# Kernel optimization log

Measured on AMD Instinct MI355X. Metric: run time of the kernel, lower is better.

The kernel has to match this reference:

```python
import jax, jax.numpy as jnp
import numpy as np

# dims: batch, tokens, model dim, heads, head_dim, context len, n_blocks, ffn dim
B, L, D, H, HD, S, NB, DFF = 1, 3072, 1024, 16, 64, 512, 2, 4096
T3, H3, W3 = 12, 16, 16  # latent video grid, T3*H3*W3 == L


def _ln(x):
    # LayerNorm, elementwise_affine=False, eps=1e-6
    m = jnp.mean(x, axis=-1, keepdims=True)
    v = jnp.mean(jnp.square(x - m), axis=-1, keepdims=True)
    return (x - m) * jax.lax.rsqrt(v + 1e-6)


def _rot_half(x):
    x1, x2 = jnp.split(x, 2, axis=-1)
    return jnp.concatenate([-x2, x1], axis=-1)


def _rope3d(head_dim, t, h, w):
    d = head_dim // 6
    def band(n):
        freqs = 1.0 / 10000.0 ** (np.arange(0, 2 * d, 2, dtype=np.float32) / (2 * d))
        return np.outer(np.arange(n, dtype=np.float32), freqs)  # [n, d]
    te, he, we = band(t), band(h), band(w)
    rope = np.zeros((t, h, w, head_dim), dtype=np.float32)
    rope[:, :, :, :d] = te[:, None, None, :]
    rope[:, :, :, d:2 * d] = he[None, :, None, :]
    rope[:, :, :, 2 * d:3 * d] = we[None, None, :, :]
    return jnp.asarray(rope.reshape(t * h * w, head_dim))


def _forward(x, timestep_emb, context_emb, rope_emb, adaW, adab, sqW, skW, svW,
             soW, sob, cqW, ckW, cvW, coW, cob, f1W, f1b, f2W, f2b):
    Bv, Lv, Dv = x.shape
    hd = rope_emb.shape[-1]
    nh = Dv // hd
    scale = hd ** -0.5
    cos = jnp.cos(rope_emb)[None, None]  # [1,1,L,hd]
    sin = jnp.sin(rope_emb)[None, None]

    def heads(y):  # [B,N,D] -> [B,H,N,hd]
        return y.reshape(Bv, -1, nh, hd).transpose(0, 2, 1, 3)

    def merge(y):  # [B,H,L,hd] -> [B,L,D]
        return y.transpose(0, 2, 1, 3).reshape(Bv, Lv, Dv)

    for i in range(adaW.shape[0]):
        mods = timestep_emb @ adaW[i].T + adab[i]  # [B, 6D]
        sh_msa, sc_msa, g_msa, sh_mlp, sc_mlp, g_mlp = jnp.split(mods, 6, axis=-1)
        # --- AdaLN + self-attention with RoPE ---
        hx = _ln(x) * (1.0 + sc_msa[:, None, :]) + sh_msa[:, None, :]
        q, k, v = heads(hx @ sqW[i].T), heads(hx @ skW[i].T), heads(hx @ svW[i].T)
        q = q * cos + _rot_half(q) * sin
        k = k * cos + _rot_half(k) * sin
        a = jax.nn.softmax(jnp.einsum('bhld,bhmd->bhlm', q, k) * scale, axis=-1)
        o = merge(jnp.einsum('bhlm,bhmd->bhld', a, v))
        x = x + g_msa[:, None, :] * (o @ soW[i].T + sob[i])
        # --- cross-attention (no gate, no modulation) ---
        hx = _ln(x)
        q = heads(hx @ cqW[i].T)
        k = heads(context_emb @ ckW[i].T)
        v = heads(context_emb @ cvW[i].T)
        a = jax.nn.softmax(jnp.einsum('bhld,bhsd->bhls', q, k) * scale, axis=-1)
        o = merge(jnp.einsum('bhls,bhsd->bhld', a, v))
        x = x + (o @ coW[i].T + cob[i])
        # --- AdaLN + MLP (exact GELU) ---
        hx = _ln(x) * (1.0 + sc_mlp[:, None, :]) + sh_mlp[:, None, :]
        hx = jax.nn.gelu(hx @ f1W[i].T + f1b[i], approximate=False)
        x = x + g_mlp[:, None, :] * (hx @ f2W[i].T + f2b[i])
    return x


def setup_inputs() -> dict:
    ks = jax.random.split(jax.random.key(0), 20)
    s = 0.02
    return {
        'x': jax.random.normal(ks[0], (B, L, D), jnp.float32),
        'timestep_emb': jax.random.normal(ks[1], (B, D), jnp.float32),
        'context_emb': jax.random.normal(ks[2], (B, S, D), jnp.float32),
        'rope_emb': _rope3d(HD, T3, H3, W3),
        'adaW': jax.random.normal(ks[3], (NB, 6 * D, D), jnp.float32) * s,
        'adab': jnp.zeros((NB, 6 * D), jnp.float32),
        'sqW': jax.random.normal(ks[4], (NB, D, D), jnp.float32) * s,
        'skW': jax.random.normal(ks[5], (NB, D, D), jnp.float32) * s,
        'svW': jax.random.normal(ks[6], (NB, D, D), jnp.float32) * s,
        'soW': jax.random.normal(ks[7], (NB, D, D), jnp.float32) * s,
        'sob': jnp.zeros((NB, D), jnp.float32),
        'cqW': jax.random.normal(ks[8], (NB, D, D), jnp.float32) * s,
        'ckW': jax.random.normal(ks[9], (NB, D, D), jnp.float32) * s,
        'cvW': jax.random.normal(ks[10], (NB, D, D), jnp.float32) * s,
        'coW': jax.random.normal(ks[11], (NB, D, D), jnp.float32) * s,
        'cob': jnp.zeros((NB, D), jnp.float32),
        'f1W': jax.random.normal(ks[12], (NB, DFF, D), jnp.float32) * s,
        'f1b': jnp.zeros((NB, DFF), jnp.float32),
        'f2W': jax.random.normal(ks[13], (NB, D, DFF), jnp.float32) * s,
        'f2b': jnp.zeros((NB, D), jnp.float32),
    }


def reference(x, timestep_emb, context_emb, rope_emb, adaW, adab, sqW, skW, svW,
              soW, sob, cqW, ckW, cvW, coW, cob, f1W, f1b, f2W, f2b):
    return _forward(x, timestep_emb, context_emb, rope_emb, adaW, adab, sqW, skW,
                    svW, soW, sob, cqW, ckW, cvW, coW, cob, f1W, f1b, f2W, f2b)
```

## Files before the change

kernel.cpp:

```cpp
#include <hip/hip_runtime.h>
#include <math.h>

typedef __attribute__((ext_vector_type(8))) short bf16x8;
typedef __attribute__((ext_vector_type(4))) float f32x4;
typedef unsigned short u16;
typedef unsigned int u32;

#define DEV static __device__ __forceinline__

typedef __attribute__((address_space(3))) u32 lds_u32;
typedef const __attribute__((address_space(1))) u32 glb_u32;

DEV void gload16(const void* g, void* l){
  __builtin_amdgcn_global_load_lds((glb_u32*)g, (lds_u32*)l, 16, 0, 0);
}

DEV u16 f2bf(float f){
  u32 u = __builtin_bit_cast(u32, f);
  u32 r = (u + 0x7fffu + ((u >> 16) & 1u)) >> 16;
  return (u16)r;
}
DEV float bf2f(u16 h){
  u32 u = ((u32)h) << 16;
  return __builtin_bit_cast(float, u);
}
DEV u32 cvtpk(float a, float b){
  u32 r;
  asm("v_cvt_pk_bf16_f32 %0, %1, %2" : "=v"(r) : "v"(a), "v"(b));
  return r;
}
DEV float gelu_exact(float x){ return 0.5f*x*(1.f+erff(x*0.70710678118654752f)); }

#define QSCALE 0.18033688f

DEV void xcd_remap(int &bx, int &by){
  int gx = gridDim.x, gy = gridDim.y;
  int n = gx*gy;
  if ((n & 7) == 0){
    int id = by*gx + bx;
    int q = n >> 3;
    int sid = (id & 7)*q + (id >> 3);
    bx = sid % gx;
    by = sid / gx;
  }
}

__global__ __launch_bounds__(256) void k_copy_f32(const float* __restrict__ in, float* __restrict__ out, int n4){
  int i = blockIdx.x*256 + threadIdx.x;
  if (i < n4) ((float4*)out)[i] = ((const float4*)in)[i];
}

__global__ __launch_bounds__(256) void k_cvt_bf16(const float* __restrict__ in, u16* __restrict__ out, int n4){
  int i = blockIdx.x*256 + threadIdx.x;
  if (i < n4){
    float4 v = ((const float4*)in)[i];
    ushort4 o;
    o.x = f2bf(v.x); o.y = f2bf(v.y); o.z = f2bf(v.z); o.w = f2bf(v.w);
    ((ushort4*)out)[i] = o;
  }
}

struct CvtArgs { const float4* s[16]; ushort4* d[16]; };
__global__ __launch_bounds__(256) void k_cvt_all(CvtArgs a){
  int i = blockIdx.x*256 + threadIdx.x;
  int seg = i >> 19;
  int off = i & 0x7FFFF;
  float4 v = a.s[seg][off];
  ushort4 o;
  o.x = f2bf(v.x); o.y = f2bf(v.y); o.z = f2bf(v.z); o.w = f2bf(v.w);
  a.d[seg][off] = o;
}

__global__ __launch_bounds__(256) void k_trig(const float* __restrict__ rope,
    float2* __restrict__ ctq, float2* __restrict__ ctk){
  int i = blockIdx.x*256 + threadIdx.x;
  int d = i & 63;
  float a = rope[i];
  float c = cosf(a), s = sinf(a);
  float sg = (d < 32) ? -s : s;
  ctk[i] = make_float2(c, sg);
  ctq[i] = make_float2(c*QSCALE, sg*QSCALE);
}

__global__ __launch_bounds__(256) void k_ada(const float* __restrict__ te,
    const float* __restrict__ adaW, const float* __restrict__ adab,
    float* __restrict__ mods){
  int row = blockIdx.x*4 + (threadIdx.x>>6);
  int lane = threadIdx.x & 63;
  const float* wr = adaW + (size_t)row*1024;
  float s = 0.f;
  #pragma unroll
  for (int j=0; j<4; j++){
    int c = lane*4 + j*256;
    float4 a = *(const float4*)(te + c);
    float4 b = *(const float4*)(wr + c);
    s += a.x*b.x + a.y*b.y + a.z*b.z + a.w*b.w;
  }
  #pragma unroll
  for (int off=32; off; off>>=1) s += __shfl_down(s, off);
  if (!lane) mods[row] = s + adab[row];
}

__global__ __launch_bounds__(256) void k_ln_mod(const float* __restrict__ x,
    const float* __restrict__ sh, const float* __restrict__ sc,
    u16* __restrict__ out){
  int row = blockIdx.x, t = threadIdx.x;
  const float* xr = x + (size_t)row*1024;
  float4 v = ((const float4*)xr)[t];
  float s  = v.x+v.y+v.z+v.w;
  float sq = v.x*v.x+v.y*v.y+v.z*v.z+v.w*v.w;
  #pragma unroll
  for (int off=32; off; off>>=1){ s += __shfl_down(s,off); sq += __shfl_down(sq,off); }
  __shared__ float red[8];
  int w = t>>6, lane = t&63;
  if (!lane){ red[w] = s; red[4+w] = sq; }
  __syncthreads();
  s  = red[0]+red[1]+red[2]+red[3];
  sq = red[4]+red[5]+red[6]+red[7];
  float mean = s*(1.f/1024.f);
  float var  = sq*(1.f/1024.f) - mean*mean;
  float rst  = rsqrtf(var + 1e-6f);
  float vv[4] = {v.x, v.y, v.z, v.w};
  ushort4 o;
  u16 ob[4];
  #pragma unroll
  for (int j=0;j<4;j++){
    int col = t*4+j;
    float y = (vv[j]-mean)*rst;
    if (sh) y = y*(1.f + sc[col]) + sh[col];
    ob[j] = f2bf(y);
  }
  o.x=ob[0]; o.y=ob[1]; o.z=ob[2]; o.w=ob[3];
  *(ushort4*)(out + (size_t)row*1024 + t*4) = o;
}

__global__ __launch_bounds__(256) void k_rope(u16* __restrict__ q, u16* __restrict__ k,
    const float* __restrict__ rope){
  int idx = blockIdx.x*256 + threadIdx.x;
  int d = idx & 31;
  int h = (idx >> 5) & 15;
  int p = idx >> 9;
  const float* rr = rope + (size_t)p*64;
  float a0 = rr[d], a1 = rr[d+32];
  float c0 = cosf(a0), s0 = sinf(a0);
  float c1 = cosf(a1), s1 = sinf(a1);
  size_t o = (size_t)p*1024 + h*64 + d;
  float q0 = bf2f(q[o]), q1 = bf2f(q[o+32]);
  q[o]    = f2bf((q0*c0 - q1*s0)*QSCALE);
  q[o+32] = f2bf((q1*c1 + q0*s1)*QSCALE);
  float k0 = bf2f(k[o]), k1 = bf2f(k[o+32]);
  k[o]    = f2bf(k0*c0 - k1*s0);
  k[o+32] = f2bf(k1*c1 + k0*s1);
}

DEV void gemm_loop(const u16* __restrict__ X, const u16* __restrict__ W,
                   int bm, int bn, int ld, int lenK, u16* As, u16* Bs, f32x4 acc[4][4])
{
  int t = threadIdx.x;
  int w = t>>6, lane = t&63;
  int wr = (w>>1)*64, wc = (w&1)*64;
  int fr = lane&15, g = lane>>4;
  int arow = lane>>2, acol = (lane&3)*8;
  const u16* xp = X + (size_t)(bm + w*32 + arow)*ld + acol;
  const u16* wp = W + (size_t)(bn + w*32 + arow)*ld + acol;
  int nk = lenK >> 5;
  {
    u16* a = As + w*1024; u16* b = Bs + w*1024;
    gload16(xp, a);             gload16(xp + (size_t)16*ld, a + 512);
    gload16(wp, b);             gload16(wp + (size_t)16*ld, b + 512);
  }
  for (int kt = 0; kt < nk; ++kt){
    __syncthreads();
    int cur = kt & 1;
    if (kt + 1 < nk){
      int nb = cur ^ 1;
      int k0 = (kt+1) << 5;
      u16* a = As + nb*4096 + w*1024; u16* b = Bs + nb*4096 + w*1024;
      gload16(xp + k0, a);        gload16(xp + k0 + (size_t)16*ld, a + 512);
      gload16(wp + k0, b);        gload16(wp + k0 + (size_t)16*ld, b + 512);
    }
    const u16* ab = As + cur*4096;
    const u16* bb = Bs + cur*4096;
    bf16x8 a[4], b[4];
    #pragma unroll
    for (int i=0;i<4;i++) a[i] = *(const bf16x8*)(ab + (wr+i*16+fr)*32 + g*8);
    #pragma unroll
    for (int i=0;i<4;i++) b[i] = *(const bf16x8*)(bb + (wc+i*16+fr)*32 + g*8);
    __builtin_amdgcn_s_setprio(1);
    #pragma unroll
    for (int i=0;i<4;i++)
      #pragma unroll
      for (int j=0;j<4;j++)
        acc[i][j] = __builtin_amdgcn_mfma_f32_16x16x32_bf16(a[i], b[j], acc[i][j], 0, 0, 0);
    __builtin_amdgcn_s_setprio(0);
  }
}

template<int EPI>
__global__ __launch_bounds__(256) void k_gemm_bf16(
    const u16* __restrict__ X, const u16* __restrict__ W,
    const float* __restrict__ bias,
    u16* __restrict__ Yout,
    const float* __restrict__ resin, float* __restrict__ resout,
    const float* __restrict__ gate,
    int M, int N, int K)
{
  __shared__ __align__(16) u16 As[2*128*32];
  __shared__ __align__(16) u16 Bs[2*128*32];
  int bx = blockIdx.x, by = blockIdx.y;
  xcd_remap(bx, by);
  int bm = bx*128, bn = by*128;
  f32x4 acc[4][4] = {};
  gemm_loop(X, W, bm, bn, K, K, As, Bs, acc);
  int lane = threadIdx.x & 63, w = threadIdx.x>>6;
  int wr = (w>>1)*64, wc = (w&1)*64;
  int fr = lane&15, g = lane>>4;
  #pragma unroll
  for (int i=0;i<4;i++){
    #pragma unroll
    for (int j=0;j<4;j++){
      int col = bn + wc + j*16 + fr;
      float bv = bias ? bias[col] : 0.f;
      #pragma unroll
      for (int r=0;r<4;r++){
        int row = bm + wr + i*16 + g*4 + r;
        float y = acc[i][j][r] + bv;
        if (EPI == 1){
          Yout[(size_t)row*N + col] = f2bf(gelu_exact(y));
        } else if (EPI == 2){
          float gt = gate ? gate[col] : 1.f;
          resout[(size_t)row*N + col] = resin[(size_t)row*N + col] + gt*y;
        } else {
          Yout[(size_t)row*N + col] = f2bf(y*QSCALE);
        }
      }
    }
  }
}

__global__ __launch_bounds__(256) void k_gemm_part(
    const u16* __restrict__ X, const u16* __restrict__ W,
    float* __restrict__ pp, int M, int N, int K, int Ks)
{
  __shared__ __align__(16) u16 As[2*128*32];
  __shared__ __align__(16) u16 Bs[2*128*32];
  int bx = blockIdx.x, by = blockIdx.y;
  xcd_remap(bx, by);
  int s = blockIdx.z;
  int bm = bx*128, bn = by*128;
  f32x4 acc[4][4] = {};
  gemm_loop(X + (size_t)s*Ks, W + (size_t)s*Ks, bm, bn, K, Ks, As, Bs, acc);
  float* out = pp + (size_t)s*M*N;
  int lane = threadIdx.x & 63, w = threadIdx.x>>6;
  int wr = (w>>1)*64, wc = (w&1)*64;
  int fr = lane&15, g = lane>>4;
  #pragma unroll
  for (int i=0;i<4;i++)
    #pragma unroll
    for (int j=0;j<4;j++){
      int col = bn + wc + j*16 + fr;
      #pragma unroll
      for (int r=0;r<4;r++){
        int row = bm + wr + i*16 + g*4 + r;
        out[(size_t)row*N + col] = acc[i][j][r];
      }
    }
}

template<int EPI>
__global__ __launch_bounds__(256) void k_reduce(
    const float* __restrict__ pp, int S, const float* __restrict__ bias,
    const float* __restrict__ resin, float* __restrict__ resout,
    const float* __restrict__ gate, u16* __restrict__ Ybf,
    int MN, int N)
{
  int idx = blockIdx.x*256 + threadIdx.x;
  int base = idx*4;
  if (base >= MN) return;
  float4 s4 = *(const float4*)(pp + base);
  for (int s=1; s<S; ++s){
    float4 t4 = *(const float4*)(pp + (size_t)s*MN + base);
    s4.x += t4.x; s4.y += t4.y; s4.z += t4.z; s4.w += t4.w;
  }
  int col = base & (N-1);
  float b0=0,b1=0,b2=0,b3=0;
  if (bias){ b0=bias[col]; b1=bias[col+1]; b2=bias[col+2]; b3=bias[col+3]; }
  if (EPI == 2){
    float g0=1,g1=1,g2=1,g3=1;
    if (gate){ g0=gate[col]; g1=gate[col+1]; g2=gate[col+2]; g3=gate[col+3]; }
    float4 rv = *(const float4*)(resin + base);
    float4 o;
    o.x = rv.x + g0*(s4.x+b0);
    o.y = rv.y + g1*(s4.y+b1);
    o.z = rv.z + g2*(s4.z+b2);
    o.w = rv.w + g3*(s4.w+b3);
    *(float4*)(resout + base) = o;
  } else {
    ushort4 o;
    o.x = f2bf((s4.x+b0)*QSCALE);
    o.y = f2bf((s4.y+b1)*QSCALE);
    o.z = f2bf((s4.z+b2)*QSCALE);
    o.w = f2bf((s4.w+b3)*QSCALE);
    *(ushort4*)(Ybf + base) = o;
  }
}

template<int MOD>
__global__ __launch_bounds__(256) void k_reduce_ln(
    const float* __restrict__ pp, int S, const float* __restrict__ bias,
    const float* __restrict__ resin, float* __restrict__ resout,
    const float* __restrict__ gate,
    const float* __restrict__ sh, const float* __restrict__ sc,
    u16* __restrict__ hx)
{
  int row = blockIdx.x, t = threadIdx.x;
  size_t base = (size_t)row*1024 + t*4;
  const size_t MN = (size_t)3072*1024;
  float4 s4 = *(const float4*)(pp + base);
  for (int s=1; s<S; ++s){
    float4 t4 = *(const float4*)(pp + (size_t)s*MN + base);
    s4.x += t4.x; s4.y += t4.y; s4.z += t4.z; s4.w += t4.w;
  }
  int col = t*4;
  float b0=0,b1=0,b2=0,b3=0;
  if (bias){ b0=bias[col]; b1=bias[col+1]; b2=bias[col+2]; b3=bias[col+3]; }
  float g0=1,g1=1,g2=1,g3=1;
  if (gate){ g0=gate[col]; g1=gate[col+1]; g2=gate[col+2]; g3=gate[col+3]; }
  float4 rv = *(const float4*)(resin + base);
  float y[4];
  y[0] = rv.x + g0*(s4.x+b0);
  y[1] = rv.y + g1*(s4.y+b1);
  y[2] = rv.z + g2*(s4.z+b2);
  y[3] = rv.w + g3*(s4.w+b3);
  float4 ov; ov.x=y[0]; ov.y=y[1]; ov.z=y[2]; ov.w=y[3];
  *(float4*)(resout + base) = ov;
  float s  = y[0]+y[1]+y[2]+y[3];
  float sq = y[0]*y[0]+y[1]*y[1]+y[2]*y[2]+y[3]*y[3];
  #pragma unroll
  for (int off=32; off; off>>=1){ s += __shfl_down(s,off); sq += __shfl_down(sq,off); }
  __shared__ float red[8];
  int w = t>>6, lane = t&63;
  if (!lane){ red[w] = s; red[4+w] = sq; }
  __syncthreads();
  s  = red[0]+red[1]+red[2]+red[3];
  sq = red[4]+red[5]+red[6]+red[7];
  float mean = s*(1.f/1024.f);
  float var  = sq*(1.f/1024.f) - mean*mean;
  float rst  = rsqrtf(var + 1e-6f);
  ushort4 o;
  u16 ob[4];
  #pragma unroll
  for (int j=0;j<4;j++){
    float yy = (y[j]-mean)*rst;
    if (MOD) yy = yy*(1.f + sc[col+j]) + sh[col+j];
    ob[j] = f2bf(yy);
  }
  o.x=ob[0]; o.y=ob[1]; o.z=ob[2]; o.w=ob[3];
  *(ushort4*)(hx + base) = o;
}

template<int MODE>
__global__ __launch_bounds__(256) void k_qkv(
    const u16* __restrict__ X,
    const u16* __restrict__ W0, const u16* __restrict__ W1, const u16* __restrict__ W2,
    u16* __restrict__ Y0, u16* __restrict__ Y1, u16* __restrict__ VT,
    const float2* __restrict__ ctq, const float2* __restrict__ ctk,
    int M, int ldvt)
{
  __shared__ __align__(16) u16 As[2*128*32];
  __shared__ __align__(16) u16 Bs[2*128*32];
  int bx = blockIdx.x, by = blockIdx.y;
  xcd_remap(bx, by);
  int bm = bx*128, bn = by*128;
  int sel = bn >> 10;
  int bnl = bn & 1023;
  const u16* W = (MODE==0) ? (sel==0 ? W0 : (sel==1 ? W1 : W2))
                           : (sel==0 ? W0 : W1);
  f32x4 acc[4][4] = {};
  gemm_loop(X, W, bm, bnl, 1024, 1024, As, Bs, acc);
  int lane = threadIdx.x & 63, w = threadIdx.x>>6;
  int wr = (w>>1)*64, wc = (w&1)*64;
  int fr = lane&15, g = lane>>4;
  const int lastSel = (MODE==0) ? 2 : 1;
  if (sel < lastSel){
    u16* Y = (sel==0) ? Y0 : Y1;
    if (MODE==0){
      const float2* ct = (sel==0) ? ctq : ctk;
      #pragma unroll
      for (int i=0;i<4;i++)
        #pragma unroll
        for (int j=0;j<4;j++){
          int col = bnl + wc + j*16 + fr;
          int d = j*16 + fr;
          #pragma unroll
          for (int r=0;r<4;r++){
            int row = bm + wr + i*16 + g*4 + r;
            float2 cs = ct[row*64 + d];
            float yv = acc[i][j][r]*cs.x + acc[i][j^2][r]*cs.y;
            Y[(size_t)row*1024 + col] = f2bf(yv);
          }
        }
    } else {
      #pragma unroll
      for (int i=0;i<4;i++)
        #pragma unroll
        for (int j=0;j<4;j++){
          int col = bnl + wc + j*16 + fr;
          #pragma unroll
          for (int r=0;r<4;r++){
            int row = bm + wr + i*16 + g*4 + r;
            Y[(size_t)row*1024 + col] = f2bf(acc[i][j][r]);
          }
        }
    }
  } else {
    #pragma unroll
    for (int i=0;i<4;i++)
      #pragma unroll
      for (int j=0;j<4;j++){
        int col = bnl + wc + j*16 + fr;
        int row0 = bm + wr + i*16 + g*4;
        uint2 pk;
        pk.x = cvtpk(acc[i][j][0], acc[i][j][1]);
        pk.y = cvtpk(acc[i][j][2], acc[i][j][3]);
        *(uint2*)(VT + (size_t)col*ldvt + row0) = pk;
      }
  }
}

template<int EPI>
__global__ __launch_bounds__(256) void k_gemm_f32(
    const u16* __restrict__ X, const float* __restrict__ W,
    const float* __restrict__ bias,
    u16* __restrict__ Yout,
    const float* __restrict__ resin, float* __restrict__ resout,
    const float* __restrict__ gate,
    int M, int N, int K)
{
  __shared__ __align__(16) u16 As[128][32];
  __shared__ __align__(16) u16 Bs[128][40];
  int bx = blockIdx.x, by = blockIdx.y;
  xcd_remap(bx, by);
  int bm = bx*128, bn = by*128;
  int t = threadIdx.x;
  int w = t>>6, lane = t&63;
  int wr = (w>>1)*64, wc = (w&1)*64;
  int fr = lane&15, g = lane>>4;
  f32x4 acc[4][4] = {};
  int arow = lane>>2, acol = (lane&3)*8;
  int srow = t>>2, scol = (t&3)*8;
  for (int k0=0; k0<K; k0+=32){
    #pragma unroll
    for (int inst=0; inst<2; ++inst){
      int r = w*32 + inst*16 + arow;
      gload16(X + (size_t)(bm+r)*K + k0 + acol, &As[w*32+inst*16][0]);
    }
    #pragma unroll
    for (int it=0; it<2; ++it){
      const float* wp = W + (size_t)(bn+srow+it*64)*K + k0 + scol;
      float4 f0 = *(const float4*)(wp);
      float4 f1 = *(const float4*)(wp+4);
      uint4 bw;
      bw.x = (u32)f2bf(f0.x) | ((u32)f2bf(f0.y)<<16);
      bw.y = (u32)f2bf(f0.z) | ((u32)f2bf(f0.w)<<16);
      bw.z = (u32)f2bf(f1.x) | ((u32)f2bf(f1.y)<<16);
      bw.w = (u32)f2bf(f1.z) | ((u32)f2bf(f1.w)<<16);
      *(uint4*)&Bs[srow+it*64][scol] = bw;
    }
    __syncthreads();
    bf16x8 a[4], b[4];
    #pragma unroll
    for (int i=0;i<4;i++) a[i] = *(const bf16x8*)&As[wr+i*16+fr][g*8];
    #pragma unroll
    for (int i=0;i<4;i++) b[i] = *(const bf16x8*)&Bs[wc+i*16+fr][g*8];
    #pragma unroll
    for (int i=0;i<4;i++)
      #pragma unroll
      for (int j=0;j<4;j++)
        acc[i][j] = __builtin_amdgcn_mfma_f32_16x16x32_bf16(a[i], b[j], acc[i][j], 0, 0, 0);
    __syncthreads();
  }
  #pragma unroll
  for (int i=0;i<4;i++){
    #pragma unroll
    for (int j=0;j<4;j++){
      int col = bn + wc + j*16 + fr;
      float bv = bias ? bias[col] : 0.f;
      #pragma unroll
      for (int r=0;r<4;r++){
        int row = bm + wr + i*16 + g*4 + r;
        float y = acc[i][j][r] + bv;
        if (EPI == 0){
          Yout[(size_t)row*N + col] = f2bf(y);
        } else if (EPI == 1){
          Yout[(size_t)row*N + col] = f2bf(gelu_exact(y));
        } else if (EPI == 2){
          float gt = gate ? gate[col] : 1.f;
          resout[(size_t)row*N + col] = resin[(size_t)row*N + col] + gt*y;
        } else if (EPI == 3){
          Yout[(size_t)col*M + row] = f2bf(y);
        } else {
          Yout[(size_t)row*N + col] = f2bf(y*QSCALE);
        }
      }
    }
  }
}

__global__ __launch_bounds__(256) void k_flash(
    const u16* __restrict__ Q, const u16* __restrict__ Kb, const u16* __restrict__ VT,
    u16* __restrict__ O, int Lkv)
{
  __shared__ __align__(16) u16 Ks[2*64*64];
  __shared__ __align__(16) u16 Vs[2*64*64];
  __shared__ __align__(16) u16 Ps[4][16][72];
  int bx = blockIdx.x, by = blockIdx.y;
  xcd_remap(bx, by);
  int h = by;
  int q0 = bx*64;
  int t = threadIdx.x, w = t>>6, lane = t&63;
  int fr = lane&15, g = lane>>4;
  const u16* qrow = Q + (size_t)(q0 + w*16 + fr)*1024 + h*64;
  bf16x8 aq0 = *(const bf16x8*)(qrow + g*8);
  bf16x8 aq1 = *(const bf16x8*)(qrow + 32 + g*8);
  f32x4 accO[4] = {};
  float l = 0.f;
  int slot = lane & 7, rop = lane >> 3;
  const u16* kbase = Kb + (size_t)h*64;
  const u16* vbase = VT + (size_t)h*64*Lkv;
  int nt = Lkv >> 6;
  {
    #pragma unroll
    for (int inst=0; inst<2; ++inst){
      int row = w*16 + inst*8 + rop;
      int ss = slot ^ (row & 7);
      gload16(kbase + (size_t)row*1024 + ss*8, Ks + (w*16+inst*8)*64);
      gload16(vbase + (size_t)row*Lkv + ss*8, Vs + (w*16+inst*8)*64);
    }
  }
  for (int tt=0; tt<nt; ++tt){
    __syncthreads();
    int cur = tt & 1;
    if (tt+1 < nt){
      int nb = cur ^ 1;
      int k0 = (tt+1) << 6;
      #pragma unroll
      for (int inst=0; inst<2; ++inst){
        int row = w*16 + inst*8 + rop;
        int ss = slot ^ (row & 7);
        gload16(kbase + (size_t)(k0+row)*1024 + ss*8, Ks + nb*4096 + (w*16+inst*8)*64);
        gload16(vbase + (size_t)row*Lkv + k0 + ss*8, Vs + nb*4096 + (w*16+inst*8)*64);
      }
    }
    const u16* kc = Ks + cur*4096;
    const u16* vc = Vs + cur*4096;
    f32x4 st[4] = {};
    __builtin_amdgcn_s_setprio(1);
    #pragma unroll
    for (int kb=0;kb<4;kb++){
      int rowK = kb*16 + fr;
      bf16x8 b0 = *(const bf16x8*)(kc + rowK*64 + ((g  ) ^ (rowK&7))*8);
      bf16x8 b1 = *(const bf16x8*)(kc + rowK*64 + ((4+g) ^ (rowK&7))*8);
      st[kb] = __builtin_amdgcn_mfma_f32_16x16x32_bf16(b0, aq0, st[kb], 0,0,0);
      st[kb] = __builtin_amdgcn_mfma_f32_16x16x32_bf16(b1, aq1, st[kb], 0,0,0);
    }
    __builtin_amdgcn_s_setprio(0);
    float ts = 0.f;
    u32 pk[8];
    #pragma unroll
    for (int kb=0;kb<4;kb++){
      float p0 = exp2f(st[kb][0]);
      float p1 = exp2f(st[kb][1]);
      float p2 = exp2f(st[kb][2]);
      float p3 = exp2f(st[kb][3]);
      ts += (p0+p1)+(p2+p3);
      pk[kb*2]   = cvtpk(p0,p1);
      pk[kb*2+1] = cvtpk(p2,p3);
    }
    ts += __shfl_xor(ts, 16);
    ts += __shfl_xor(ts, 32);
    l += ts;
    #pragma unroll
    for (int kb=0;kb<4;kb++){
      uint2 pv; pv.x = pk[kb*2]; pv.y = pk[kb*2+1];
      *(uint2*)&Ps[w][fr][kb*16 + g*4] = pv;
    }
    bf16x8 ap0 = *(const bf16x8*)&Ps[w][fr][g*8];
    bf16x8 ap1 = *(const bf16x8*)&Ps[w][fr][32 + g*8];
    __builtin_amdgcn_s_setprio(1);
    #pragma unroll
    for (int nd=0; nd<4; nd++){
      int rowV = nd*16 + fr;
      bf16x8 b0 = *(const bf16x8*)(vc + rowV*64 + ((g  ) ^ (rowV&7))*8);
      bf16x8 b1 = *(const bf16x8*)(vc + rowV*64 + ((4+g) ^ (rowV&7))*8);
      accO[nd] = __builtin_amdgcn_mfma_f32_16x16x32_bf16(ap0, b0, accO[nd], 0,0,0);
      accO[nd] = __builtin_amdgcn_mfma_f32_16x16x32_bf16(ap1, b1, accO[nd], 0,0,0);
    }
    __builtin_amdgcn_s_setprio(0);
  }
  float rl = 1.f / l;
  #pragma unroll
  for (int r=0;r<4;r++){
    float rlq = __shfl(rl, g*4+r);
    int row = q0 + w*16 + g*4 + r;
    #pragma unroll
    for (int nd=0; nd<4; nd++)
      O[(size_t)row*1024 + h*64 + nd*16 + fr] = f2bf(accO[nd][r] * rlq);
  }
}

extern "C" void kernel_launch(void* const* d_in, const int* in_sizes, int n_in,
                              void* d_out, int out_size, void* d_ws, size_t ws_size,
                              hipStream_t stream){
  const float* x_in = (const float*)d_in[0];
  const float* te   = (const float*)d_in[1];
  const float* ctx  = (const float*)d_in[2];
  const float* rope = (const float*)d_in[3];
  const float* adaW = (const float*)d_in[4];
  const float* adab = (const float*)d_in[5];
  const float* sqW  = (const float*)d_in[6];
  const float* skW  = (const float*)d_in[7];
  const float* svW  = (const float*)d_in[8];
  const float* soW  = (const float*)d_in[9];
  const float* sob  = (const float*)d_in[10];
  const float* cqW  = (const float*)d_in[11];
  const float* ckW  = (const float*)d_in[12];
  const float* cvW  = (const float*)d_in[13];
  const float* coW  = (const float*)d_in[14];
  const float* cob  = (const float*)d_in[15];
  const float* f1W  = (const float*)d_in[16];
  const float* f1b  = (const float*)d_in[17];
  const float* f2W  = (const float*)d_in[18];
  const float* f2b  = (const float*)d_in[19];
  float* x = (float*)d_out;

  char* p = (char*)d_ws;
  size_t used = 0;
  auto alloc = [&](size_t bytes){
    void* r = (void*)(p + used);
    used += (bytes + 255) & ~(size_t)255;
    return r;
  };
  u16* hx   = (u16*)alloc((size_t)3072*1024*2);
  u16* qb   = (u16*)alloc((size_t)3072*1024*2);
  u16* kb   = (u16*)alloc((size_t)3072*1024*2);
  u16* vt   = (u16*)alloc((size_t)1024*3072*2);
  u16* ob   = (u16*)alloc((size_t)3072*1024*2);
  u16* mid  = (u16*)alloc((size_t)3072*4096*2);
  u16* ctxb = (u16*)alloc((size_t)512*1024*2);
  float* mods = (float*)alloc((size_t)2*6144*4);
  float2* ctq = (float2*)alloc((size_t)3072*64*8);
  float2* ctk = (float2*)alloc((size_t)3072*64*8);
  size_t base_used = used;
  const size_t NW_SMALL = (size_t)2*1024*1024;
  const size_t NW_BIG   = (size_t)2*4096*1024;
  size_t wbytes = (8*NW_SMALL + 2*NW_BIG)*2;
  bool pre = (base_used + wbytes + 4096) <= ws_size;

  u16 *sqWb=nullptr,*skWb=nullptr,*svWb=nullptr,*soWb=nullptr,
      *cqWb=nullptr,*ckWb=nullptr,*cvWb=nullptr,*coWb=nullptr,
      *f1Wb=nullptr,*f2Wb=nullptr;
  if (pre){
    sqWb=(u16*)alloc(NW_SMALL*2); skWb=(u16*)alloc(NW_SMALL*2);
    svWb=(u16*)alloc(NW_SMALL*2); soWb=(u16*)alloc(NW_SMALL*2);
    cqWb=(u16*)alloc(NW_SMALL*2); ckWb=(u16*)alloc(NW_SMALL*2);
    cvWb=(u16*)alloc(NW_SMALL*2); coWb=(u16*)alloc(NW_SMALL*2);
    f1Wb=(u16*)alloc(NW_BIG*2);   f2Wb=(u16*)alloc(NW_BIG*2);
  }
  const size_t PPN = (size_t)4*3072*1024;
  float* pp = nullptr;
  bool splitok = pre && (used + PPN*4 + 4096) <= ws_size;
  if (splitok) pp = (float*)alloc(PPN*4);
  const int MN = 3072*1024;

  if (pre){
    CvtArgs ca;
    const float* smallW[8] = {sqW,skW,svW,soW,cqW,ckW,cvW,coW};
    u16* smallD[8] = {sqWb,skWb,svWb,soWb,cqWb,ckWb,cvWb,coWb};
    for (int s=0; s<8; ++s){ ca.s[s] = (const float4*)smallW[s]; ca.d[s] = (ushort4*)smallD[s]; }
    for (int qd=0; qd<4; ++qd){
      ca.s[8+qd]  = (const float4*)f1W + (size_t)qd*524288;
      ca.d[8+qd]  = (ushort4*)f1Wb + (size_t)qd*524288;
      ca.s[12+qd] = (const float4*)f2W + (size_t)qd*524288;
      ca.d[12+qd] = (ushort4*)f2Wb + (size_t)qd*524288;
    }
    k_cvt_all<<<32768, 256, 0, stream>>>(ca);
  }
  k_cvt_bf16<<<512, 256, 0, stream>>>(ctx, ctxb, 131072);
  k_ada<<<3072, 256, 0, stream>>>(te, adaW, adab, mods);
  k_trig<<<768, 256, 0, stream>>>(rope, ctq, ctk);
  if (!splitok) k_copy_f32<<<3072, 256, 0, stream>>>(x_in, x, 786432);

  for (int i=0; i<2; ++i){
    const float* mi  = mods + (size_t)i*6144;
    const float* mi2 = mods + 6144;
    size_t wo = (size_t)i*1024*1024;
    size_t wof = (size_t)i*4096*1024;
    if (i == 0 || !splitok)
      k_ln_mod<<<3072,256,0,stream>>>(i==0 ? x_in : x, mi+0, mi+1024, hx);
    if (pre){
      k_qkv<0><<<dim3(24,24),256,0,stream>>>(hx, sqWb+wo, skWb+wo, svWb+wo, qb, kb, vt, ctq, ctk, 3072, 3072);
    } else {
      k_gemm_f32<0><<<dim3(24,8),256,0,stream>>>(hx, sqW+wo, nullptr, qb, nullptr,nullptr,nullptr, 3072,1024,1024);
      k_gemm_f32<0><<<dim3(24,8),256,0,stream>>>(hx, skW+wo, nullptr, kb, nullptr,nullptr,nullptr, 3072,1024,1024);
      k_gemm_f32<3><<<dim3(24,8),256,0,stream>>>(hx, svW+wo, nullptr, vt, nullptr,nullptr,nullptr, 3072,1024,1024);
      k_rope<<<6144,256,0,stream>>>(qb, kb, rope);
    }
    k_flash<<<dim3(48,16),256,0,stream>>>(qb, kb, vt, ob, 3072);
    if (splitok){
      k_gemm_part<<<dim3(24,8,2),256,0,stream>>>(ob, soWb+wo, pp, 3072,1024,1024,512);
      k_reduce_ln<0><<<3072,256,0,stream>>>(pp, 2, sob+(size_t)i*1024,
          (i==0 ? x_in : (const float*)x), x, mi+2048, nullptr, nullptr, hx);
    } else if (pre){
      k_gemm_bf16<2><<<dim3(24,8),256,0,stream>>>(ob, soWb+wo, sob+(size_t)i*1024, nullptr, x, x, mi+2048, 3072,1024,1024);
      k_ln_mod<<<3072,256,0,stream>>>(x, nullptr, nullptr, hx);
    } else {
      k_gemm_f32<2><<<dim3(24,8),256,0,stream>>>(ob, soW+wo, sob+(size_t)i*1024, nullptr, x, x, mi+2048, 3072,1024,1024);
      k_ln_mod<<<3072,256,0,stream>>>(x, nullptr, nullptr, hx);
    }
    if (splitok){
      k_gemm_part<<<dim3(24,8,2),256,0,stream>>>(hx, cqWb+wo, pp, 3072,1024,1024,512);
      k_reduce<4><<<3072,256,0,stream>>>(pp, 2, nullptr, nullptr, nullptr, nullptr, qb, MN, 1024);
      k_qkv<1><<<dim3(4,16),256,0,stream>>>(ctxb, ckWb+wo, cvWb+wo, nullptr, kb, nullptr, vt, nullptr, nullptr, 512, 512);
    } else if (pre){
      k_gemm_bf16<4><<<dim3(24,8),256,0,stream>>>(hx, cqWb+wo, nullptr, qb, nullptr,nullptr,nullptr, 3072,1024,1024);
      k_qkv<1><<<dim3(4,16),256,0,stream>>>(ctxb, ckWb+wo, cvWb+wo, nullptr, kb, nullptr, vt, nullptr, nullptr, 512, 512);
    } else {
      k_gemm_f32<4><<<dim3(24,8),256,0,stream>>>(hx, cqW+wo, nullptr, qb, nullptr,nullptr,nullptr, 3072,1024,1024);
      k_gemm_f32<0><<<dim3(4,8),256,0,stream>>>(ctxb, ckW+wo, nullptr, kb, nullptr,nullptr,nullptr, 512,1024,1024);
      k_gemm_f32<3><<<dim3(4,8),256,0,stream>>>(ctxb, cvW+wo, nullptr, vt, nullptr,nullptr,nullptr, 512,1024,1024);
    }
    k_flash<<<dim3(48,16),256,0,stream>>>(qb, kb, vt, ob, 512);
    if (splitok){
      k_gemm_part<<<dim3(24,8,2),256,0,stream>>>(ob, coWb+wo, pp, 3072,1024,1024,512);
      k_reduce_ln<1><<<3072,256,0,stream>>>(pp, 2, cob+(size_t)i*1024, x, x, nullptr, mi+3072, mi+4096, hx);
    } else if (pre){
      k_gemm_bf16<2><<<dim3(24,8),256,0,stream>>>(ob, coWb+wo, cob+(size_t)i*1024, nullptr, x, x, nullptr, 3072,1024,1024);
      k_ln_mod<<<3072,256,0,stream>>>(x, mi+3072, mi+4096, hx);
    } else {
      k_gemm_f32<2><<<dim3(24,8),256,0,stream>>>(ob, coW+wo, cob+(size_t)i*1024, nullptr, x, x, nullptr, 3072,1024,1024);
      k_ln_mod<<<3072,256,0,stream>>>(x, mi+3072, mi+4096, hx);
    }
    if (pre){
      k_gemm_bf16<1><<<dim3(24,32),256,0,stream>>>(hx, f1Wb+wof, f1b+(size_t)i*4096, mid, nullptr,nullptr,nullptr, 3072,4096,1024);
    } else {
      k_gemm_f32<1><<<dim3(24,32),256,0,stream>>>(hx, f1W+wof, f1b+(size_t)i*4096, mid, nullptr,nullptr,nullptr, 3072,4096,1024);
    }
    if (splitok){
      k_gemm_part<<<dim3(24,8,4),256,0,stream>>>(mid, f2Wb+wof, pp, 3072,1024,4096,1024);
      if (i == 0)
        k_reduce_ln<1><<<3072,256,0,stream>>>(pp, 4, f2b, x, x, mi+5120, mi2+0, mi2+1024, hx);
      else
        k_reduce<2><<<3072,256,0,stream>>>(pp, 4, f2b+1024, x, x, mi+5120, nullptr, MN, 1024);
    } else if (pre){
      k_gemm_bf16<2><<<dim3(24,8),256,0,stream>>>(mid, f2Wb+wof, f2b+(size_t)i*1024, nullptr, x, x, mi+5120, 3072,1024,4096);
    } else {
      k_gemm_f32<2><<<dim3(24,8),256,0,stream>>>(mid, f2W+wof, f2b+(size_t)i*1024, nullptr, x, x, mi+5120, 3072,1024,4096);
    }
  }
}
```

Before: 787.4 us.

## Give each flash warp two query groups and add a small-tile context KV kernel

The flash attention kernel now runs 128 threads, and each warp handles 32 query rows as two 16-row groups. Each K/V fragment loaded from LDS is therefore reused for two MFMA groups, halving LDS reads per unit of compute, at the cost of more registers and fewer waves per block. A new 64x64-tile kernel computes the cross-attention context K/V projection with 256 blocks instead of 64, so the small 512-token GEMM fills more compute units. The MODE=1 path of k_qkv is removed, since that case now goes through the new kernel.

```diff
diff --git a/kernel.cpp b/kernel.cpp
--- a/kernel.cpp
+++ b/kernel.cpp
@@ -374,45 +374,29 @@
   int bm = bx*128, bn = by*128;
   int sel = bn >> 10;
   int bnl = bn & 1023;
-  const u16* W = (MODE==0) ? (sel==0 ? W0 : (sel==1 ? W1 : W2))
-                           : (sel==0 ? W0 : W1);
+  const u16* W = (sel==0 ? W0 : (sel==1 ? W1 : W2));
   f32x4 acc[4][4] = {};
   gemm_loop(X, W, bm, bnl, 1024, 1024, As, Bs, acc);
   int lane = threadIdx.x & 63, w = threadIdx.x>>6;
   int wr = (w>>1)*64, wc = (w&1)*64;
   int fr = lane&15, g = lane>>4;
-  const int lastSel = (MODE==0) ? 2 : 1;
-  if (sel < lastSel){
+  if (sel < 2){
     u16* Y = (sel==0) ? Y0 : Y1;
-    if (MODE==0){
-      const float2* ct = (sel==0) ? ctq : ctk;
-      #pragma unroll
-      for (int i=0;i<4;i++)
+    const float2* ct = (sel==0) ? ctq : ctk;
+    #pragma unroll
+    for (int i=0;i<4;i++)
+      #pragma unroll
+      for (int j=0;j<4;j++){
+        int col = bnl + wc + j*16 + fr;
+        int d = j*16 + fr;
         #pragma unroll
-        for (int j=0;j<4;j++){
-          int col = bnl + wc + j*16 + fr;
-          int d = j*16 + fr;
-          #pragma unroll
-          for (int r=0;r<4;r++){
-            int row = bm + wr + i*16 + g*4 + r;
-            float2 cs = ct[row*64 + d];
-            float yv = acc[i][j][r]*cs.x + acc[i][j^2][r]*cs.y;
-            Y[(size_t)row*1024 + col] = f2bf(yv);
-          }
+        for (int r=0;r<4;r++){
+          int row = bm + wr + i*16 + g*4 + r;
+          float2 cs = ct[row*64 + d];
+          float yv = acc[i][j][r]*cs.x + acc[i][j^2][r]*cs.y;
+          Y[(size_t)row*1024 + col] = f2bf(yv);
         }
-    } else {
-      #pragma unroll
-      for (int i=0;i<4;i++)
-        #pragma unroll
-        for (int j=0;j<4;j++){
-          int col = bnl + wc + j*16 + fr;
-          #pragma unroll
-          for (int r=0;r<4;r++){
-            int row = bm + wr + i*16 + g*4 + r;
-            Y[(size_t)row*1024 + col] = f2bf(acc[i][j][r]);
-          }
-        }
-    }
+      }
   } else {
     #pragma unroll
     for (int i=0;i<4;i++)
@@ -426,6 +410,75 @@
         *(uint2*)(VT + (size_t)col*ldvt + row0) = pk;
       }
   }
+}
+
+__global__ __launch_bounds__(256) void k_kv64(
+    const u16* __restrict__ X,
+    const u16* __restrict__ Wk, const u16* __restrict__ Wv,
+    u16* __restrict__ Kout, u16* __restrict__ VTout, int ldvt)
+{
+  __shared__ __align__(16) u16 As[2*64*32];
+  __shared__ __align__(16) u16 Bs[2*64*32];
+  int bx = blockIdx.x, by = blockIdx.y;
+  xcd_remap(bx, by);
+  int bm = bx*64;
+  int sel = by >> 4;
+  int bnl = (by & 15)*64;
+  const u16* W = sel ? Wv : Wk;
+  int t = threadIdx.x, w = t>>6, lane = t&63;
+  int wr = (w>>1)*32, wc = (w&1)*32;
+  int fr = lane&15, g = lane>>4;
+  f32x4 acc[2][2] = {};
+  int arow = lane>>2, acol = (lane&3)*8;
+  const u16* xp = X + (size_t)(bm + w*16 + arow)*1024 + acol;
+  const u16* wp = W + (size_t)(bnl + w*16 + arow)*1024 + acol;
+  {
+    gload16(xp, As + w*512);
+    gload16(wp, Bs + w*512);
+  }
+  for (int kt = 0; kt < 32; ++kt){
+    __syncthreads();
+    int cur = kt & 1;
+    if (kt + 1 < 32){
+      int nb = cur ^ 1;
+      int k0 = (kt+1) << 5;
+      gload16(xp + k0, As + nb*2048 + w*512);
+      gload16(wp + k0, Bs + nb*2048 + w*512);
+    }
+    const u16* ab = As + cur*2048;
+    const u16* bb = Bs + cur*2048;
+    bf16x8 a[2], b[2];
+    #pragma unroll
+    for (int i=0;i<2;i++) a[i] = *(const bf16x8*)(ab + (wr+i*16+fr)*32 + g*8);
+    #pragma unroll
+    for (int i=0;i<2;i++) b[i] = *(const bf16x8*)(bb + (wc+i*16+fr)*32 + g*8);
+    __builtin_amdgcn_s_setprio(1);
+    #pragma unroll
+    for (int i=0;i<2;i++)
+      #pragma unroll
+      for (int j=0;j<2;j++)
+        acc[i][j] = __builtin_amdgcn_mfma_f32_16x16x32_bf16(a[i], b[j], acc[i][j], 0, 0, 0);
+    __builtin_amdgcn_s_setprio(0);
+  }
+  #pragma unroll
+  for (int i=0;i<2;i++)
+    #pragma unroll
+    for (int j=0;j<2;j++){
+      int col = bnl + wc + j*16 + fr;
+      if (sel == 0){
+        #pragma unroll
+        for (int r=0;r<4;r++){
+          int row = bm + wr + i*16 + g*4 + r;
+          Kout[(size_t)row*1024 + col] = f2bf(acc[i][j][r]);
+        }
+      } else {
+        int row0 = bm + wr + i*16 + g*4;
+        uint2 pk;
+        pk.x = cvtpk(acc[i][j][0], acc[i][j][1]);
+        pk.y = cvtpk(acc[i][j][2], acc[i][j][3]);
+        *(uint2*)(VTout + (size_t)col*ldvt + row0) = pk;
+      }
+    }
 }
 
 template<int EPI>
@@ -507,105 +560,134 @@
   }
 }
 
-__global__ __launch_bounds__(256) void k_flash(
+__global__ __launch_bounds__(128) void k_flash(
     const u16* __restrict__ Q, const u16* __restrict__ Kb, const u16* __restrict__ VT,
     u16* __restrict__ O, int Lkv)
 {
   __shared__ __align__(16) u16 Ks[2*64*64];
   __shared__ __align__(16) u16 Vs[2*64*64];
-  __shared__ __align__(16) u16 Ps[4][16][72];
+  __shared__ __align__(16) u16 Ps[2][32][72];
   int bx = blockIdx.x, by = blockIdx.y;
   xcd_remap(bx, by);
   int h = by;
   int q0 = bx*64;
   int t = threadIdx.x, w = t>>6, lane = t&63;
   int fr = lane&15, g = lane>>4;
-  const u16* qrow = Q + (size_t)(q0 + w*16 + fr)*1024 + h*64;
-  bf16x8 aq0 = *(const bf16x8*)(qrow + g*8);
-  bf16x8 aq1 = *(const bf16x8*)(qrow + 32 + g*8);
-  f32x4 accO[4] = {};
-  float l = 0.f;
+  bf16x8 aq0[2], aq1[2];
+  #pragma unroll
+  for (int qg=0; qg<2; ++qg){
+    const u16* qrow = Q + (size_t)(q0 + w*32 + qg*16 + fr)*1024 + h*64;
+    aq0[qg] = *(const bf16x8*)(qrow + g*8);
+    aq1[qg] = *(const bf16x8*)(qrow + 32 + g*8);
+  }
+  f32x4 accO[2][4] = {};
+  float l0 = 0.f, l1 = 0.f;
   int slot = lane & 7, rop = lane >> 3;
   const u16* kbase = Kb + (size_t)h*64;
   const u16* vbase = VT + (size_t)h*64*Lkv;
   int nt = Lkv >> 6;
-  {
-    #pragma unroll
-    for (int inst=0; inst<2; ++inst){
-      int row = w*16 + inst*8 + rop;
+  auto stage = [&](int tt, int buf){
+    int k0 = tt << 6;
+    #pragma unroll
+    for (int ps=0; ps<4; ++ps){
+      int row = ps*16 + w*8 + rop;
       int ss = slot ^ (row & 7);
-      gload16(kbase + (size_t)row*1024 + ss*8, Ks + (w*16+inst*8)*64);
-      gload16(vbase + (size_t)row*Lkv + ss*8, Vs + (w*16+inst*8)*64);
-    }
-  }
+      gload16(kbase + (size_t)(k0+row)*1024 + ss*8, Ks + buf*4096 + row*64);
+      gload16(vbase + (size_t)row*Lkv + k0 + ss*8, Vs + buf*4096 + row*64);
+    }
+  };
+  stage(0, 0);
   for (int tt=0; tt<nt; ++tt){
     __syncthreads();
     int cur = tt & 1;
-    if (tt+1 < nt){
-      int nb = cur ^ 1;
-      int k0 = (tt+1) << 6;
-      #pragma unroll
-      for (int inst=0; inst<2; ++inst){
-        int row = w*16 + inst*8 + rop;
-        int ss = slot ^ (row & 7);
-        gload16(kbase + (size_t)(k0+row)*1024 + ss*8, Ks + nb*4096 + (w*16+inst*8)*64);
-        gload16(vbase + (size_t)row*Lkv + k0 + ss*8, Vs + nb*4096 + (w*16+inst*8)*64);
-      }
-    }
+    if (tt+1 < nt) stage(tt+1, cur^1);
     const u16* kc = Ks + cur*4096;
     const u16* vc = Vs + cur*4096;
-    f32x4 st[4] = {};
+    f32x4 st0[4] = {}, st1[4] = {};
     __builtin_amdgcn_s_setprio(1);
     #pragma unroll
     for (int kb=0;kb<4;kb++){
       int rowK = kb*16 + fr;
-      bf16x8 b0 = *(const bf16x8*)(kc + rowK*64 + ((g  ) ^ (rowK&7))*8);
-      bf16x8 b1 = *(const bf16x8*)(kc + rowK*64 + ((4+g) ^ (rowK&7))*8);
-      st[kb] = __builtin_amdgcn_mfma_f32_16x16x32_bf16(b0, aq0, st[kb], 0,0,0);
-      st[kb] = __builtin_amdgcn_mfma_f32_16x16x32_bf16(b1, aq1, st[kb], 0,0,0);
+      bf16x8 kA0 = *(const bf16x8*)(kc + rowK*64 + ((g  ) ^ (rowK&7))*8);
+      bf16x8 kA1 = *(const bf16x8*)(kc + rowK*64 + ((4+g) ^ (rowK&7))*8);
+      st0[kb] = __builtin_amdgcn_mfma_f32_16x16x32_bf16(kA0, aq0[0], st0[kb], 0,0,0);
+      st0[kb] = __builtin_amdgcn_mfma_f32_16x16x32_bf16(kA1, aq1[0], st0[kb], 0,0,0);
+      st1[kb] = __builtin_amdgcn_mfma_f32_16x16x32_bf16(kA0, aq0[1], st1[kb], 0,0,0);
+      st1[kb] = __builtin_amdgcn_mfma_f32_16x16x32_bf16(kA1, aq1[1], st1[kb], 0,0,0);
     }
     __builtin_amdgcn_s_setprio(0);
-    float ts = 0.f;
-    u32 pk[8];
-    #pragma unroll
-    for (int kb=0;kb<4;kb++){
-      float p0 = exp2f(st[kb][0]);
-      float p1 = exp2f(st[kb][1]);
-      float p2 = exp2f(st[kb][2]);
-      float p3 = exp2f(st[kb][3]);
-      ts += (p0+p1)+(p2+p3);
-      pk[kb*2]   = cvtpk(p0,p1);
-      pk[kb*2+1] = cvtpk(p2,p3);
-    }
-    ts += __shfl_xor(ts, 16);
-    ts += __shfl_xor(ts, 32);
-    l += ts;
-    #pragma unroll
-    for (int kb=0;kb<4;kb++){
-      uint2 pv; pv.x = pk[kb*2]; pv.y = pk[kb*2+1];
-      *(uint2*)&Ps[w][fr][kb*16 + g*4] = pv;
-    }
-    bf16x8 ap0 = *(const bf16x8*)&Ps[w][fr][g*8];
-    bf16x8 ap1 = *(const bf16x8*)&Ps[w][fr][32 + g*8];
+    {
+      float ts = 0.f;
+      u32 pk[8];
+      #pragma unroll
+      for (int kb=0;kb<4;kb++){
+        float p0 = exp2f(st0[kb][0]);
+        float p1 = exp2f(st0[kb][1]);
+        float p2 = exp2f(st0[kb][2]);
+        float p3 = exp2f(st0[kb][3]);
+        ts += (p0+p1)+(p2+p3);
+        pk[kb*2]   = cvtpk(p0,p1);
+        pk[kb*2+1] = cvtpk(p2,p3);
+      }
+      ts += __shfl_xor(ts, 16);
+      ts += __shfl_xor(ts, 32);
+      l0 += ts;
+      #pragma unroll
+      for (int kb=0;kb<4;kb++){
+        uint2 pv; pv.x = pk[kb*2]; pv.y = pk[kb*2+1];
+        *(uint2*)&Ps[w][fr][kb*16 + g*4] = pv;
+      }
+    }
+    {
+      float ts = 0.f;
+      u32 pk[8];
+      #pragma unroll
+      for (int kb=0;kb<4;kb++){
+        float p0 = exp2f(st1[kb][0]);
+        float p1 = exp2f(st1[kb][1]);
+        float p2 = exp2f(st1[kb][2]);
+        float p3 = exp2f(st1[kb][3]);
+        ts += (p0+p1)+(p2+p3);
+        pk[kb*2]   = cvtpk(p0,p1);
+        pk[kb*2+1] = cvtpk(p2,p3);
+      }
+      ts += __shfl_xor(ts, 16);
+      ts += __shfl_xor(ts, 32);
+      l1 += ts;
+      #pragma unroll
+      for (int kb=0;kb<4;kb++){
+        uint2 pv; pv.x = pk[kb*2]; pv.y = pk[kb*2+1];
+        *(uint2*)&Ps[w][16+fr][kb*16 + g*4] = pv;
+      }
+    }
+    bf16x8 ap0g0 = *(const bf16x8*)&Ps[w][fr][g*8];
+    bf16x8 ap1g0 = *(const bf16x8*)&Ps[w][fr][32 + g*8];
+    bf16x8 ap0g1 = *(const bf16x8*)&Ps[w][16+fr][g*8];
+    bf16x8 ap1g1 = *(const bf16x8*)&Ps[w][16+fr][32 + g*8];
     __builtin_amdgcn_s_setprio(1);
     #pragma unroll
     for (int nd=0; nd<4; nd++){
       int rowV = nd*16 + fr;
-      bf16x8 b0 = *(const bf16x8*)(vc + rowV*64 + ((g  ) ^ (rowV&7))*8);
-      bf16x8 b1 = *(const bf16x8*)(vc + rowV*64 + ((4+g) ^ (rowV&7))*8);
-      accO[nd] = __builtin_amdgcn_mfma_f32_16x16x32_bf16(ap0, b0, accO[nd], 0,0,0);
-      accO[nd] = __builtin_amdgcn_mfma_f32_16x16x32_bf16(ap1, b1, accO[nd], 0,0,0);
+      bf16x8 vB0 = *(const bf16x8*)(vc + rowV*64 + ((g  ) ^ (rowV&7))*8);
+      bf16x8 vB1 = *(const bf16x8*)(vc + rowV*64 + ((4+g) ^ (rowV&7))*8);
+      accO[0][nd] = __builtin_amdgcn_mfma_f32_16x16x32_bf16(ap0g0, vB0, accO[0][nd], 0,0,0);
+      accO[0][nd] = __builtin_amdgcn_mfma_f32_16x16x32_bf16(ap1g0, vB1, accO[0][nd], 0,0,0);
+      accO[1][nd] = __builtin_amdgcn_mfma_f32_16x16x32_bf16(ap0g1, vB0, accO[1][nd], 0,0,0);
+      accO[1][nd] = __builtin_amdgcn_mfma_f32_16x16x32_bf16(ap1g1, vB1, accO[1][nd], 0,0,0);
     }
     __builtin_amdgcn_s_setprio(0);
   }
-  float rl = 1.f / l;
-  #pragma unroll
-  for (int r=0;r<4;r++){
-    float rlq = __shfl(rl, g*4+r);
-    int row = q0 + w*16 + g*4 + r;
-    #pragma unroll
-    for (int nd=0; nd<4; nd++)
-      O[(size_t)row*1024 + h*64 + nd*16 + fr] = f2bf(accO[nd][r] * rlq);
+  #pragma unroll
+  for (int qg=0; qg<2; ++qg){
+    float rl = 1.f / (qg ? l1 : l0);
+    #pragma unroll
+    for (int r=0;r<4;r++){
+      float rlq = __shfl(rl, g*4+r);
+      int row = q0 + w*32 + qg*16 + g*4 + r;
+      #pragma unroll
+      for (int nd=0; nd<4; nd++)
+        O[(size_t)row*1024 + h*64 + nd*16 + fr] = f2bf(accO[qg][nd][r] * rlq);
+    }
   }
 }
 
@@ -706,7 +788,7 @@
       k_gemm_f32<3><<<dim3(24,8),256,0,stream>>>(hx, svW+wo, nullptr, vt, nullptr,nullptr,nullptr, 3072,1024,1024);
       k_rope<<<6144,256,0,stream>>>(qb, kb, rope);
     }
-    k_flash<<<dim3(48,16),256,0,stream>>>(qb, kb, vt, ob, 3072);
+    k_flash<<<dim3(48,16),128,0,stream>>>(qb, kb, vt, ob, 3072);
     if (splitok){
       k_gemm_part<<<dim3(24,8,2),256,0,stream>>>(ob, soWb+wo, pp, 3072,1024,1024,512);
       k_reduce_ln<0><<<3072,256,0,stream>>>(pp, 2, sob+(size_t)i*1024,
@@ -721,16 +803,16 @@
     if (splitok){
       k_gemm_part<<<dim3(24,8,2),256,0,stream>>>(hx, cqWb+wo, pp, 3072,1024,1024,512);
       k_reduce<4><<<3072,256,0,stream>>>(pp, 2, nullptr, nullptr, nullptr, nullptr, qb, MN, 1024);
-      k_qkv<1><<<dim3(4,16),256,0,stream>>>(ctxb, ckWb+wo, cvWb+wo, nullptr, kb, nullptr, vt, nullptr, nullptr, 512, 512);
+      k_kv64<<<dim3(8,32),256,0,stream>>>(ctxb, ckWb+wo, cvWb+wo, kb, vt, 512);
     } else if (pre){
       k_gemm_bf16<4><<<dim3(24,8),256,0,stream>>>(hx, cqWb+wo, nullptr, qb, nullptr,nullptr,nullptr, 3072,1024,1024);
-      k_qkv<1><<<dim3(4,16),256,0,stream>>>(ctxb, ckWb+wo, cvWb+wo, nullptr, kb, nullptr, vt, nullptr, nullptr, 512, 512);
+      k_kv64<<<dim3(8,32),256,0,stream>>>(ctxb, ckWb+wo, cvWb+wo, kb, vt, 512);
     } else {
       k_gemm_f32<4><<<dim3(24,8),256,0,stream>>>(hx, cqW+wo, nullptr, qb, nullptr,nullptr,nullptr, 3072,1024,1024);
       k_gemm_f32<0><<<dim3(4,8),256,0,stream>>>(ctxb, ckW+wo, nullptr, kb, nullptr,nullptr,nullptr, 512,1024,1024);
       k_gemm_f32<3><<<dim3(4,8),256,0,stream>>>(ctxb, cvW+wo, nullptr, vt, nullptr,nullptr,nullptr, 512,1024,1024);
     }
-    k_flash<<<dim3(48,16),256,0,stream>>>(qb, kb, vt, ob, 512);
+    k_flash<<<dim3(48,16),128,0,stream>>>(qb, kb, vt, ob, 512);
     if (splitok){
       k_gemm_part<<<dim3(24,8,2),256,0,stream>>>(ob, coWb+wo, pp, 3072,1024,1024,512);
       k_reduce_ln<1><<<3072,256,0,stream>>>(pp, 2, cob+(size_t)i*1024, x, x, nullptr, mi+3072, mi+4096, hx);
```

After: 816.0 us. 1.04x slower.
